# Performance work log

Measured on AMD Instinct MI355X. Metric: run time of the kernel, lower is better.

Reference implementation:

```python
import jax, jax.numpy as jnp
import numpy as np

N_NODES = 100000
N_EDGES = 1600000
IN_F, HID_F, OUT_F, N_CLS = 128, 64, 16, 5
EPS = 1e-12


def _glorot(key, shape):
    fan_in, fan_out = shape[0], shape[1]
    lim = float(np.sqrt(6.0 / (fan_in + fan_out)))
    return jax.random.uniform(key, shape, jnp.float32, -lim, lim)


def setup_inputs() -> dict:
    key = jax.random.key(0)
    ks = jax.random.split(key, 12)
    x = jax.random.normal(ks[0], (N_NODES, IN_F), jnp.float32)
    src = jax.random.randint(ks[1], (N_EDGES,), 0, N_NODES)
    dst = jax.random.randint(ks[2], (N_EDGES,), 0, N_NODES)
    return {
        "x": x, "src": src, "dst": dst,
        # conv1 (SAGEConv pool): fc_pool [in,in]+bias, fc_self/fc_neigh [in,hid] no bias, shared bias
        "pool1_W": _glorot(ks[3], (IN_F, IN_F)), "pool1_b": jnp.zeros((IN_F,), jnp.float32),
        "self1_W": _glorot(ks[4], (IN_F, HID_F)), "neigh1_W": _glorot(ks[5], (IN_F, HID_F)),
        "bias1": jnp.zeros((HID_F,), jnp.float32),
        # conv2
        "pool2_W": _glorot(ks[6], (HID_F, HID_F)), "pool2_b": jnp.zeros((HID_F,), jnp.float32),
        "self2_W": _glorot(ks[7], (HID_F, OUT_F)), "neigh2_W": _glorot(ks[8], (HID_F, OUT_F)),
        "bias2": jnp.zeros((OUT_F,), jnp.float32),
        # edge predictor: Linear(2*out, 5)
        "pred_W": _glorot(ks[9], (2 * OUT_F, N_CLS)), "pred_b": jnp.zeros((N_CLS,), jnp.float32),
    }


def _sage_pool_conv(h, src, dst, Wp, bp, Ws, Wn, b):
    # pool aggregator: m = relu(fc_pool(h)); h_neigh[v] = max over in-edges of m[src]
    m = jax.nn.relu(h @ Wp + bp)                        # [N, d]
    agg = jax.ops.segment_max(m[src], dst, num_segments=h.shape[0])  # [N, d]
    agg = jnp.where(jnp.isneginf(agg), 0.0, agg)        # zero for isolated nodes (DGL behavior)
    return h @ Ws + agg @ Wn + b


def _norm_relu(h):
    # torch F.normalize(p=2, dim=1, eps=1e-12) then relu
    n = jnp.sqrt(jnp.sum(h * h, axis=1, keepdims=True))
    return jax.nn.relu(h / jnp.maximum(n, EPS))


def reference(x, src, dst, pool1_W, pool1_b, self1_W, neigh1_W, bias1,
              pool2_W, pool2_b, self2_W, neigh2_W, bias2, pred_W, pred_b):
    h = _sage_pool_conv(x, src, dst, pool1_W, pool1_b, self1_W, neigh1_W, bias1)
    h = _norm_relu(h)
    h = _sage_pool_conv(h, src, dst, pool2_W, pool2_b, self2_W, neigh2_W, bias2)
    h = _norm_relu(h)                                   # [N, OUT_F]
    # edge scorer: W @ concat(h_u, h_v) + b, split W to avoid materializing concat
    W_u, W_v = pred_W[:OUT_F], pred_W[OUT_F:]
    score = h[src] @ W_u + h[dst] @ W_v + pred_b        # [E, 5]
    return score
```

## Files before the change

kernel.cpp:

```cpp
#include <hip/hip_runtime.h>

#define N_NODES 100000
#define N_EDGES 1600000
constexpr int IN_F = 128, HID_F = 64, OUT_F = 16, N_CLS = 5;

constexpr int NPB = 128;
constexpr int NBK = (N_NODES + NPB - 1) / NPB;
constexpr int BCAP = 2400;
constexpr int FCH = 4096;
constexpr int NCH = (N_EDGES + FCH - 1) / FCH;

typedef __attribute__((ext_vector_type(8))) short bf16x8;
typedef __attribute__((ext_vector_type(4))) float f32x4;
typedef __attribute__((ext_vector_type(2))) unsigned short u16x2;

__device__ __forceinline__ float bf_lo(unsigned u) {
  return __uint_as_float(u << 16);
}
__device__ __forceinline__ float bf_hi(unsigned u) {
  return __uint_as_float(u & 0xffff0000u);
}
__device__ __forceinline__ unsigned f2bf(float f) {
  unsigned u = __float_as_uint(f);
  return (u + 0x7fffu + ((u >> 16) & 1u)) >> 16;
}
__device__ __forceinline__ void unpack8(uint4 u, float* f) {
  f[0] = bf_lo(u.x); f[1] = bf_hi(u.x);
  f[2] = bf_lo(u.y); f[3] = bf_hi(u.y);
  f[4] = bf_lo(u.z); f[5] = bf_hi(u.z);
  f[6] = bf_lo(u.w); f[7] = bf_hi(u.w);
}

__device__ __forceinline__ unsigned pkmax(unsigned a, unsigned b) {
  const u16x2 r = __builtin_elementwise_max(__builtin_bit_cast(u16x2, a),
                                            __builtin_bit_cast(u16x2, b));
  return __builtin_bit_cast(unsigned, r);
}
__device__ __forceinline__ uint4 pkmax4(uint4 a, uint4 b) {
  a.x = pkmax(a.x, b.x);
  a.y = pkmax(a.y, b.y);
  a.z = pkmax(a.z, b.z);
  a.w = pkmax(a.w, b.w);
  return a;
}

template <int K1, int FOUT, bool TWO, bool X1BF, bool X2BF, bool NORM,
          bool YBF>
__global__ __launch_bounds__(256) void node_gemm_mfma(
    const void* __restrict__ X1, const void* __restrict__ X2,
    const float* __restrict__ W1, const float* __restrict__ W2,
    const float* __restrict__ B, void* __restrict__ Y, int n) {
  constexpr int KT = 64;
  constexpr int KT2 = KT / 2;
  constexpr int NT1 = K1 / KT;
  constexpr int NT = TWO ? 2 * NT1 : NT1;
  constexpr int NFT = FOUT / 16;
  constexpr int BM = 64;
  __shared__ unsigned xt[BM * KT2];
  __shared__ unsigned wt[FOUT * KT2];

  const int tid = threadIdx.x;
  const int base = blockIdx.x * BM;
  const int wave = tid >> 6, lane = tid & 63;
  const int l15 = lane & 15, l4 = lane >> 4;

  f32x4 acc[NFT];
#pragma unroll
  for (int nt = 0; nt < NFT; ++nt) {
    const float b = B[nt * 16 + l15];
    acc[nt] = {b, b, b, b};
  }

  for (int t = 0; t < NT; ++t) {
    const bool second = TWO && t >= NT1;
    const int kt0 = (t % NT1) * KT;
#pragma unroll
    for (int q = 0; q < BM * KT2 / 256; ++q) {
      const int idx = tid + q * 256;
      const int r = idx >> 5, c2 = idx & 31;
      const int node = base + r;
      unsigned pk = 0;
      if (node < n) {
        if (second) {
          if (X2BF) {
            pk = reinterpret_cast<const unsigned*>(
                X2)[(size_t)node * (K1 / 2) + kt0 / 2 + c2];
          } else {
            const float2 f2 = reinterpret_cast<const float2*>(
                X2)[(size_t)node * (K1 / 2) + kt0 / 2 + c2];
            pk = f2bf(f2.x) | (f2bf(f2.y) << 16);
          }
        } else {
          if (X1BF) {
            pk = reinterpret_cast<const unsigned*>(
                X1)[(size_t)node * (K1 / 2) + kt0 / 2 + c2];
          } else {
            const float2 f2 = reinterpret_cast<const float2*>(
                X1)[(size_t)node * (K1 / 2) + kt0 / 2 + c2];
            pk = f2bf(f2.x) | (f2bf(f2.y) << 16);
          }
        }
      }
      xt[r * KT2 + (c2 ^ ((r & 7) << 2))] = pk;
    }
    {
      const float* __restrict__ Ws = second ? W2 : W1;
#pragma unroll
      for (int q = 0; q < FOUT * KT2 / 256; ++q) {
        const int idx = tid + q * 256;
        const int c2 = idx / FOUT, f = idx % FOUT;
        const float w0 = Ws[(size_t)(kt0 + 2 * c2) * FOUT + f];
        const float w1 = Ws[(size_t)(kt0 + 2 * c2 + 1) * FOUT + f];
        wt[f * KT2 + (c2 ^ ((f & 7) << 2))] = f2bf(w0) | (f2bf(w1) << 16);
      }
    }
    __syncthreads();
#pragma unroll
    for (int ks = 0; ks < 2; ++ks) {
      const int ar = wave * 16 + l15;
      const bf16x8 af = *reinterpret_cast<const bf16x8*>(
          &xt[ar * KT2 + (((ks * 4 + l4) ^ (l15 & 7)) << 2)]);
#pragma unroll
      for (int nt = 0; nt < NFT; ++nt) {
        const int f = nt * 16 + l15;
        const bf16x8 bfr = *reinterpret_cast<const bf16x8*>(
            &wt[f * KT2 + (((ks * 4 + l4) ^ (l15 & 7)) << 2)]);
        acc[nt] =
            __builtin_amdgcn_mfma_f32_16x16x32_bf16(af, bfr, acc[nt], 0, 0, 0);
      }
    }
    __syncthreads();
  }

  if (NORM) {
    float ss[4] = {0.f, 0.f, 0.f, 0.f};
#pragma unroll
    for (int nt = 0; nt < NFT; ++nt)
#pragma unroll
      for (int r = 0; r < 4; ++r) ss[r] += acc[nt][r] * acc[nt][r];
#pragma unroll
    for (int r = 0; r < 4; ++r) {
#pragma unroll
      for (int off = 1; off < 16; off <<= 1) ss[r] += __shfl_xor(ss[r], off, 16);
      ss[r] = 1.0f / fmaxf(sqrtf(ss[r]), 1e-12f);
    }
#pragma unroll
    for (int nt = 0; nt < NFT; ++nt)
#pragma unroll
      for (int r = 0; r < 4; ++r) acc[nt][r] = fmaxf(acc[nt][r] * ss[r], 0.f);
  } else {
#pragma unroll
    for (int nt = 0; nt < NFT; ++nt)
#pragma unroll
      for (int r = 0; r < 4; ++r) acc[nt][r] = fmaxf(acc[nt][r], 0.f);
  }
#pragma unroll
  for (int r = 0; r < 4; ++r) {
    const int node = base + wave * 16 + l4 * 4 + r;
    if (node < n) {
#pragma unroll
      for (int nt = 0; nt < NFT; ++nt) {
        if (YBF)
          reinterpret_cast<unsigned short*>(Y)[(size_t)node * FOUT + nt * 16 +
                                               l15] =
              (unsigned short)f2bf(acc[nt][r]);
        else
          reinterpret_cast<float*>(Y)[(size_t)node * FOUT + nt * 16 + l15] =
              acc[nt][r];
      }
    }
  }
}

__global__ __launch_bounds__(256) void bucket_fill(
    const int* __restrict__ src, const int* __restrict__ dst,
    int* __restrict__ cursor, unsigned* __restrict__ bedges) {
  __shared__ int hist[NBK];
  __shared__ int bbase[NBK];
  const int tid = threadIdx.x;
  const int c0 = blockIdx.x * FCH;
  const int n4 = (min(FCH, N_EDGES - c0)) >> 2;
  for (int i = tid; i < NBK; i += 256) hist[i] = 0;
  __syncthreads();
  const int4* __restrict__ s4 = reinterpret_cast<const int4*>(src + c0);
  const int4* __restrict__ d4 = reinterpret_cast<const int4*>(dst + c0);
  int4 sv[4], dv[4];
#pragma unroll
  for (int q = 0; q < 4; ++q) {
    const int i = tid + q * 256;
    if (i < n4) {
      sv[q] = s4[i];
      dv[q] = d4[i];
      atomicAdd(&hist[dv[q].x >> 7], 1);
      atomicAdd(&hist[dv[q].y >> 7], 1);
      atomicAdd(&hist[dv[q].z >> 7], 1);
      atomicAdd(&hist[dv[q].w >> 7], 1);
    }
  }
  __syncthreads();
  for (int i = tid; i < NBK; i += 256) {
    const int c = hist[i];
    bbase[i] = c ? atomicAdd(&cursor[i], c) : 0;
    hist[i] = 0;
  }
  __syncthreads();
#pragma unroll
  for (int q = 0; q < 4; ++q) {
    const int i = tid + q * 256;
    if (i < n4) {
#define PUT(dd, ss)                                        \
  {                                                        \
    const int b_ = (dd) >> 7;                              \
    const int r_ = bbase[b_] + atomicAdd(&hist[b_], 1);    \
    if (r_ < BCAP)                                         \
      bedges[(size_t)b_ * BCAP + r_] =                     \
          (unsigned)(ss) | ((unsigned)((dd) & 127) << 20); \
  }
      PUT(dv[q].x, sv[q].x)
      PUT(dv[q].y, sv[q].y)
      PUT(dv[q].z, sv[q].z)
      PUT(dv[q].w, sv[q].w)
#undef PUT
    }
  }
}

__global__ __launch_bounds__(256) void bucket_sort(unsigned* __restrict__ bedges,
                                                   const int* __restrict__ cnt,
                                                   int* __restrict__ ninfo) {
  __shared__ unsigned el[BCAP];
  __shared__ unsigned el2[BCAP];
  __shared__ int hist[NPB];
  __shared__ int csum[NPB];
  __shared__ int posl[NPB];
  const int b = blockIdx.x;
  const int n = min(cnt[b], BCAP);
  unsigned* __restrict__ bp = bedges + (size_t)b * BCAP;
  for (int i = threadIdx.x; i < n; i += 256) el[i] = bp[i];
  for (int i = threadIdx.x; i < NPB; i += 256) hist[i] = 0;
  __syncthreads();
  for (int i = threadIdx.x; i < n; i += 256) atomicAdd(&hist[el[i] >> 20], 1);
  __syncthreads();
  if (threadIdx.x < NPB) csum[threadIdx.x] = hist[threadIdx.x];
  __syncthreads();
  for (int off = 1; off < NPB; off <<= 1) {
    int u = 0;
    if (threadIdx.x < NPB && threadIdx.x >= off) u = csum[threadIdx.x - off];
    __syncthreads();
    if (threadIdx.x < NPB) csum[threadIdx.x] += u;
    __syncthreads();
  }
  if (threadIdx.x < NPB) {
    const int c = hist[threadIdx.x];
    const int beg = csum[threadIdx.x] - c;
    posl[threadIdx.x] = beg;
    const int node = b * NPB + threadIdx.x;
    if (node < N_NODES) ninfo[node] = beg | (c << 12);
  }
  __syncthreads();
  for (int i = threadIdx.x; i < n; i += 256) {
    const unsigned w = el[i];
    const int p = atomicAdd(&posl[w >> 20], 1);
    el2[p] = w & 0xFFFFF;
  }
  __syncthreads();
  for (int i = threadIdx.x; i < n; i += 256) bp[i] = el2[i];
}

template <int LPN>
__global__ __launch_bounds__(256, 8) void gather_max_pk(
    const uint4* __restrict__ M4, const int* __restrict__ ninfo,
    const int* __restrict__ sedges, uint4* __restrict__ A4) {
  constexpr int GPB = 256 / LPN;
  constexpr int UNR = 6;
  const int li = threadIdx.x % LPN;
  const int g0 = blockIdx.x * GPB + threadIdx.x / LPN;
  const int stride = gridDim.x * GPB;
  for (int node = g0; node < N_NODES; node += stride) {
    const int w = ninfo[node];
    const int cnt = w >> 12;
    uint4 a = {0u, 0u, 0u, 0u};
    if (cnt) {
      const int beg = (node >> 7) * BCAP + (w & 0xFFF);
      const int last = beg + cnt - 1;
      for (int j = beg; j <= last; j += UNR) {
        int s[UNR];
#pragma unroll
        for (int q = 0; q < UNR; ++q) s[q] = sedges[min(j + q, last)];
        uint4 u[UNR];
#pragma unroll
        for (int q = 0; q < UNR; ++q) u[q] = M4[(size_t)s[q] * LPN + li];
#pragma unroll
        for (int q = 0; q < UNR; ++q) a = pkmax4(a, u[q]);
      }
    }
    A4[(size_t)node * LPN + li] = a;
  }
}

__global__ __launch_bounds__(256) void edge_score_bf16_kernel(
    const uint4* __restrict__ H, const int* __restrict__ src,
    const int* __restrict__ dst, const float* __restrict__ PW,
    const float* __restrict__ PB, float* __restrict__ OUT) {
  __shared__ float Wl[2 * OUT_F * N_CLS];
  __shared__ float bl[N_CLS];
  if (threadIdx.x < 2 * OUT_F * N_CLS) Wl[threadIdx.x] = PW[threadIdx.x];
  if (threadIdx.x < N_CLS) bl[threadIdx.x] = PB[threadIdx.x];
  __syncthreads();
  for (int e = blockIdx.x * 256 + threadIdx.x; e < N_EDGES;
       e += gridDim.x * 256) {
    const int s = src[e], d = dst[e];
    const uint4 s0 = H[(size_t)s * 2], s1 = H[(size_t)s * 2 + 1];
    const uint4 d0 = H[(size_t)d * 2], d1 = H[(size_t)d * 2 + 1];
    float hs[OUT_F], hd[OUT_F];
    unpack8(s0, hs); unpack8(s1, hs + 8);
    unpack8(d0, hd); unpack8(d1, hd + 8);
    float acc[N_CLS];
#pragma unroll
    for (int c = 0; c < N_CLS; ++c) acc[c] = bl[c];
#pragma unroll
    for (int k = 0; k < OUT_F; ++k) {
#pragma unroll
      for (int c = 0; c < N_CLS; ++c) {
        acc[c] = fmaf(hs[k], Wl[k * N_CLS + c], acc[c]);
        acc[c] = fmaf(hd[k], Wl[(OUT_F + k) * N_CLS + c], acc[c]);
      }
    }
    float* o = OUT + (size_t)e * N_CLS;
#pragma unroll
    for (int c = 0; c < N_CLS; ++c) o[c] = acc[c];
  }
}

extern "C" void kernel_launch(void* const* d_in, const int* in_sizes, int n_in,
                              void* d_out, int out_size, void* d_ws,
                              size_t ws_size, hipStream_t stream) {
  const float* x = (const float*)d_in[0];
  const int* src = (const int*)d_in[1];
  const int* dst = (const int*)d_in[2];
  const float* pool1_W = (const float*)d_in[3];
  const float* pool1_b = (const float*)d_in[4];
  const float* self1_W = (const float*)d_in[5];
  const float* neigh1_W = (const float*)d_in[6];
  const float* bias1 = (const float*)d_in[7];
  const float* pool2_W = (const float*)d_in[8];
  const float* pool2_b = (const float*)d_in[9];
  const float* self2_W = (const float*)d_in[10];
  const float* neigh2_W = (const float*)d_in[11];
  const float* bias2 = (const float*)d_in[12];
  const float* pred_W = (const float*)d_in[13];
  const float* pred_b = (const float*)d_in[14];
  float* out = (float*)d_out;

  int* cursor = (int*)d_ws;
  int* ninfo = cursor + 1024;
  unsigned* bedges = (unsigned*)(ninfo + 100352);
  char* bufA = (char*)(bedges + (size_t)NBK * BCAP);
  char* bufB = bufA + 25600000;
  void* m1 = (void*)bufA;
  void* agg1 = (void*)bufB;
  void* h1 = (void*)bufA;
  void* m2 = (void*)bufB;
  void* agg2 = (void*)(bufA + 12800000);
  void* h2 = (void*)bufB;

  hipMemsetAsync(cursor, 0, 1024 * sizeof(int), stream);
  bucket_fill<<<NCH, 256, 0, stream>>>(src, dst, cursor, bedges);
  bucket_sort<<<NBK, 256, 0, stream>>>(bedges, cursor, ninfo);

  const int ngrid = (N_NODES + 63) / 64;

  node_gemm_mfma<IN_F, IN_F, false, false, false, false, true>
      <<<ngrid, 256, 0, stream>>>(x, nullptr, pool1_W, nullptr, pool1_b, m1,
                                  N_NODES);
  gather_max_pk<16><<<2048, 256, 0, stream>>>(
      (const uint4*)m1, ninfo, (const int*)bedges, (uint4*)agg1);
  node_gemm_mfma<IN_F, HID_F, true, false, true, true, true>
      <<<ngrid, 256, 0, stream>>>(x, agg1, self1_W, neigh1_W, bias1, h1,
                                  N_NODES);

  node_gemm_mfma<HID_F, HID_F, false, true, false, false, true>
      <<<ngrid, 256, 0, stream>>>(h1, nullptr, pool2_W, nullptr, pool2_b, m2,
                                  N_NODES);
  gather_max_pk<8><<<2048, 256, 0, stream>>>(
      (const uint4*)m2, ninfo, (const int*)bedges, (uint4*)agg2);
  node_gemm_mfma<HID_F, OUT_F, true, true, true, true, true>
      <<<ngrid, 256, 0, stream>>>(h1, agg2, self2_W, neigh2_W, bias2, h2,
                                  N_NODES);

  edge_score_bf16_kernel<<<4096, 256, 0, stream>>>((const uint4*)h2, src, dst,
                                                   pred_W, pred_b, out);
}
```

Baseline: 238.5 us.

## Store pool outputs in feature planes and gather per plane for locality

The pool GEMMs now write their bf16 output as 16-feature planes, each node's 32 bytes contiguous within a plane, instead of row-major. A new gather kernel assigns each block one plane and 128 nodes, with two lanes per node. With 8 consecutive blocks covering the same nodes across planes, each plane's working set (about 3.2 MB) is meant to fit better in L2 and the MI355X CDNA4 cache hierarchy during the random gathers. The cost is more blocks, more ninfo and edge-index reads (once per plane), and smaller 32-byte gather granules.

```diff
diff --git a/kernel.cpp b/kernel.cpp
--- a/kernel.cpp
+++ b/kernel.cpp
@@ -45,7 +45,7 @@
 }
 
 template <int K1, int FOUT, bool TWO, bool X1BF, bool X2BF, bool NORM,
-          bool YBF>
+          bool YBF, bool YPLANE>
 __global__ __launch_bounds__(256) void node_gemm_mfma(
     const void* __restrict__ X1, const void* __restrict__ X2,
     const float* __restrict__ W1, const float* __restrict__ W2,
@@ -160,13 +160,16 @@
     if (node < n) {
 #pragma unroll
       for (int nt = 0; nt < NFT; ++nt) {
-        if (YBF)
-          reinterpret_cast<unsigned short*>(Y)[(size_t)node * FOUT + nt * 16 +
-                                               l15] =
+        if (YBF) {
+          const size_t idx = YPLANE
+                                 ? ((size_t)nt * n + node) * 16 + l15
+                                 : (size_t)node * FOUT + nt * 16 + l15;
+          reinterpret_cast<unsigned short*>(Y)[idx] =
               (unsigned short)f2bf(acc[nt][r]);
-        else
+        } else {
           reinterpret_cast<float*>(Y)[(size_t)node * FOUT + nt * 16 + l15] =
               acc[nt][r];
+        }
       }
     }
   }
@@ -267,35 +270,37 @@
   for (int i = threadIdx.x; i < n; i += 256) bp[i] = el2[i];
 }
 
-template <int LPN>
-__global__ __launch_bounds__(256, 8) void gather_max_pk(
-    const uint4* __restrict__ M4, const int* __restrict__ ninfo,
+template <int NPLANES, int NSUB>
+__global__ __launch_bounds__(256) void plane_gather_max(
+    const uint4* __restrict__ MP, const int* __restrict__ ninfo,
     const int* __restrict__ sedges, uint4* __restrict__ A4) {
-  constexpr int GPB = 256 / LPN;
-  constexpr int UNR = 6;
-  const int li = threadIdx.x % LPN;
-  const int g0 = blockIdx.x * GPB + threadIdx.x / LPN;
-  const int stride = gridDim.x * GPB;
-  for (int node = g0; node < N_NODES; node += stride) {
-    const int w = ninfo[node];
-    const int cnt = w >> 12;
-    uint4 a = {0u, 0u, 0u, 0u};
-    if (cnt) {
-      const int beg = (node >> 7) * BCAP + (w & 0xFFF);
-      const int last = beg + cnt - 1;
-      for (int j = beg; j <= last; j += UNR) {
-        int s[UNR];
-#pragma unroll
-        for (int q = 0; q < UNR; ++q) s[q] = sedges[min(j + q, last)];
-        uint4 u[UNR];
-#pragma unroll
-        for (int q = 0; q < UNR; ++q) u[q] = M4[(size_t)s[q] * LPN + li];
-#pragma unroll
-        for (int q = 0; q < UNR; ++q) a = pkmax4(a, u[q]);
-      }
-    }
-    A4[(size_t)node * LPN + li] = a;
-  }
+  constexpr int UNR = 8;
+  const int s = blockIdx.x & 7;
+  const int chunk = blockIdx.x >> 3;
+  const int plane = s % NPLANES;
+  const int sub = s / NPLANES;
+  const int node = chunk * (128 * NSUB) + sub * 128 + (threadIdx.x >> 1);
+  const int li = threadIdx.x & 1;
+  if (node >= N_NODES) return;
+  const uint4* __restrict__ P = MP + (size_t)plane * N_NODES * 2;
+  const int w = ninfo[node];
+  const int cnt = w >> 12;
+  uint4 a = {0u, 0u, 0u, 0u};
+  if (cnt) {
+    const int beg = (node >> 7) * BCAP + (w & 0xFFF);
+    const int last = beg + cnt - 1;
+    for (int j = beg; j <= last; j += UNR) {
+      int ss[UNR];
+#pragma unroll
+      for (int q = 0; q < UNR; ++q) ss[q] = sedges[min(j + q, last)];
+      uint4 u[UNR];
+#pragma unroll
+      for (int q = 0; q < UNR; ++q) u[q] = P[(size_t)ss[q] * 2 + li];
+#pragma unroll
+      for (int q = 0; q < UNR; ++q) a = pkmax4(a, u[q]);
+    }
+  }
+  A4[(size_t)node * (NPLANES * 2) + plane * 2 + li] = a;
 }
 
 __global__ __launch_bounds__(256) void edge_score_bf16_kernel(
@@ -369,22 +374,24 @@
   bucket_sort<<<NBK, 256, 0, stream>>>(bedges, cursor, ninfo);
 
   const int ngrid = (N_NODES + 63) / 64;
-
-  node_gemm_mfma<IN_F, IN_F, false, false, false, false, true>
+  const int gchunks1 = (N_NODES + 127) / 128;
+  const int gchunks2 = (N_NODES + 255) / 256;
+
+  node_gemm_mfma<IN_F, IN_F, false, false, false, false, true, true>
       <<<ngrid, 256, 0, stream>>>(x, nullptr, pool1_W, nullptr, pool1_b, m1,
                                   N_NODES);
-  gather_max_pk<16><<<2048, 256, 0, stream>>>(
+  plane_gather_max<8, 1><<<gchunks1 * 8, 256, 0, stream>>>(
       (const uint4*)m1, ninfo, (const int*)bedges, (uint4*)agg1);
-  node_gemm_mfma<IN_F, HID_F, true, false, true, true, true>
+  node_gemm_mfma<IN_F, HID_F, true, false, true, true, true, false>
       <<<ngrid, 256, 0, stream>>>(x, agg1, self1_W, neigh1_W, bias1, h1,
                                   N_NODES);
 
-  node_gemm_mfma<HID_F, HID_F, false, true, false, false, true>
+  node_gemm_mfma<HID_F, HID_F, false, true, false, false, true, true>
       <<<ngrid, 256, 0, stream>>>(h1, nullptr, pool2_W, nullptr, pool2_b, m2,
                                   N_NODES);
-  gather_max_pk<8><<<2048, 256, 0, stream>>>(
+  plane_gather_max<4, 2><<<gchunks2 * 8, 256, 0, stream>>>(
       (const uint4*)m2, ninfo, (const int*)bedges, (uint4*)agg2);
-  node_gemm_mfma<HID_F, OUT_F, true, true, true, true, true>
+  node_gemm_mfma<HID_F, OUT_F, true, true, true, true, true, false>
       <<<ngrid, 256, 0, stream>>>(h1, agg2, self2_W, neigh2_W, bias2, h2,
                                   N_NODES);
 
```

Measured after the change: 294.6 us. 23.5% more time.

## Fuse self-projection into pool GEMM to avoid re-reading node features

Applied to the files above, without the earlier changes.

The pool-projection GEMM now also computes the self-projection (h @ Ws) in the same pass over the node features, storing it as bf16 in scratch space borrowed from the output buffer. The combine kernel then only multiplies the aggregated features by Wn, adds the stored self term, and applies normalize and ReLU. This removes a second read of x (fp32, 128 wide) and of h1, at the cost of writing and re-reading an extra bf16 intermediate and a wider weight tile in shared memory. Rounding the self term to bf16 before the add slightly changes numerics.

```diff
diff --git a/kernel.cpp b/kernel.cpp
--- a/kernel.cpp
+++ b/kernel.cpp
@@ -19,6 +19,9 @@
 }
 __device__ __forceinline__ float bf_hi(unsigned u) {
   return __uint_as_float(u & 0xffff0000u);
+}
+__device__ __forceinline__ float us2f(unsigned short u) {
+  return __uint_as_float(((unsigned)u) << 16);
 }
 __device__ __forceinline__ unsigned f2bf(float f) {
   unsigned u = __float_as_uint(f);
@@ -44,20 +47,20 @@
   return a;
 }
 
-template <int K1, int FOUT, bool TWO, bool X1BF, bool X2BF, bool NORM,
-          bool YBF>
-__global__ __launch_bounds__(256) void node_gemm_mfma(
-    const void* __restrict__ X1, const void* __restrict__ X2,
-    const float* __restrict__ W1, const float* __restrict__ W2,
-    const float* __restrict__ B, void* __restrict__ Y, int n) {
+template <int K1, int F1, int F2, bool XBF>
+__global__ __launch_bounds__(256) void dense_dual_mfma(
+    const void* __restrict__ X, const float* __restrict__ W1,
+    const float* __restrict__ W2, const float* __restrict__ B,
+    void* __restrict__ Y1, void* __restrict__ Y2, int n) {
   constexpr int KT = 64;
   constexpr int KT2 = KT / 2;
-  constexpr int NT1 = K1 / KT;
-  constexpr int NT = TWO ? 2 * NT1 : NT1;
-  constexpr int NFT = FOUT / 16;
+  constexpr int NT = K1 / KT;
+  constexpr int FT = F1 + F2;
+  constexpr int NFT = FT / 16;
+  constexpr int NF1 = F1 / 16;
   constexpr int BM = 64;
   __shared__ unsigned xt[BM * KT2];
-  __shared__ unsigned wt[FOUT * KT2];
+  __shared__ unsigned wt[FT * KT2];
 
   const int tid = threadIdx.x;
   const int base = blockIdx.x * BM;
@@ -67,13 +70,12 @@
   f32x4 acc[NFT];
 #pragma unroll
   for (int nt = 0; nt < NFT; ++nt) {
-    const float b = B[nt * 16 + l15];
+    const float b = (nt < NF1) ? B[nt * 16 + l15] : 0.f;
     acc[nt] = {b, b, b, b};
   }
 
   for (int t = 0; t < NT; ++t) {
-    const bool second = TWO && t >= NT1;
-    const int kt0 = (t % NT1) * KT;
+    const int kt0 = t * KT;
 #pragma unroll
     for (int q = 0; q < BM * KT2 / 256; ++q) {
       const int idx = tid + q * 256;
@@ -81,38 +83,30 @@
       const int node = base + r;
       unsigned pk = 0;
       if (node < n) {
-        if (second) {
-          if (X2BF) {
-            pk = reinterpret_cast<const unsigned*>(
-                X2)[(size_t)node * (K1 / 2) + kt0 / 2 + c2];
-          } else {
-            const float2 f2 = reinterpret_cast<const float2*>(
-                X2)[(size_t)node * (K1 / 2) + kt0 / 2 + c2];
-            pk = f2bf(f2.x) | (f2bf(f2.y) << 16);
-          }
+        if (XBF) {
+          pk = reinterpret_cast<const unsigned*>(
+              X)[(size_t)node * (K1 / 2) + kt0 / 2 + c2];
         } else {
-          if (X1BF) {
-            pk = reinterpret_cast<const unsigned*>(
-                X1)[(size_t)node * (K1 / 2) + kt0 / 2 + c2];
-          } else {
-            const float2 f2 = reinterpret_cast<const float2*>(
-                X1)[(size_t)node * (K1 / 2) + kt0 / 2 + c2];
-            pk = f2bf(f2.x) | (f2bf(f2.y) << 16);
-          }
+          const float2 f2 = reinterpret_cast<const float2*>(
+              X)[(size_t)node * (K1 / 2) + kt0 / 2 + c2];
+          pk = f2bf(f2.x) | (f2bf(f2.y) << 16);
         }
       }
       xt[r * KT2 + (c2 ^ ((r & 7) << 2))] = pk;
     }
-    {
-      const float* __restrict__ Ws = second ? W2 : W1;
-#pragma unroll
-      for (int q = 0; q < FOUT * KT2 / 256; ++q) {
-        const int idx = tid + q * 256;
-        const int c2 = idx / FOUT, f = idx % FOUT;
-        const float w0 = Ws[(size_t)(kt0 + 2 * c2) * FOUT + f];
-        const float w1 = Ws[(size_t)(kt0 + 2 * c2 + 1) * FOUT + f];
-        wt[f * KT2 + (c2 ^ ((f & 7) << 2))] = f2bf(w0) | (f2bf(w1) << 16);
-      }
+#pragma unroll
+    for (int q = 0; q < FT * KT2 / 256; ++q) {
+      const int idx = tid + q * 256;
+      const int c2 = idx / FT, f = idx % FT;
+      float w0, w1;
+      if (f < F1) {
+        w0 = W1[(size_t)(kt0 + 2 * c2) * F1 + f];
+        w1 = W1[(size_t)(kt0 + 2 * c2 + 1) * F1 + f];
+      } else {
+        w0 = W2[(size_t)(kt0 + 2 * c2) * F2 + (f - F1)];
+        w1 = W2[(size_t)(kt0 + 2 * c2 + 1) * F2 + (f - F1)];
+      }
+      wt[f * KT2 + (c2 ^ ((f & 7) << 2))] = f2bf(w0) | (f2bf(w1) << 16);
     }
     __syncthreads();
 #pragma unroll
@@ -132,41 +126,119 @@
     __syncthreads();
   }
 
-  if (NORM) {
-    float ss[4] = {0.f, 0.f, 0.f, 0.f};
-#pragma unroll
-    for (int nt = 0; nt < NFT; ++nt)
-#pragma unroll
-      for (int r = 0; r < 4; ++r) ss[r] += acc[nt][r] * acc[nt][r];
-#pragma unroll
-    for (int r = 0; r < 4; ++r) {
-#pragma unroll
-      for (int off = 1; off < 16; off <<= 1) ss[r] += __shfl_xor(ss[r], off, 16);
-      ss[r] = 1.0f / fmaxf(sqrtf(ss[r]), 1e-12f);
-    }
-#pragma unroll
-    for (int nt = 0; nt < NFT; ++nt)
-#pragma unroll
-      for (int r = 0; r < 4; ++r) acc[nt][r] = fmaxf(acc[nt][r] * ss[r], 0.f);
-  } else {
-#pragma unroll
-    for (int nt = 0; nt < NFT; ++nt)
-#pragma unroll
-      for (int r = 0; r < 4; ++r) acc[nt][r] = fmaxf(acc[nt][r], 0.f);
-  }
 #pragma unroll
   for (int r = 0; r < 4; ++r) {
     const int node = base + wave * 16 + l4 * 4 + r;
     if (node < n) {
 #pragma unroll
       for (int nt = 0; nt < NFT; ++nt) {
-        if (YBF)
-          reinterpret_cast<unsigned short*>(Y)[(size_t)node * FOUT + nt * 16 +
-                                               l15] =
+        if (nt < NF1) {
+          reinterpret_cast<unsigned short*>(Y1)[(size_t)node * F1 + nt * 16 +
+                                                l15] =
+              (unsigned short)f2bf(fmaxf(acc[nt][r], 0.f));
+        } else {
+          reinterpret_cast<unsigned short*>(Y2)[(size_t)node * F2 +
+                                                (nt - NF1) * 16 + l15] =
               (unsigned short)f2bf(acc[nt][r]);
-        else
-          reinterpret_cast<float*>(Y)[(size_t)node * FOUT + nt * 16 + l15] =
-              acc[nt][r];
+        }
+      }
+    }
+  }
+}
+
+template <int K1, int FOUT>
+__global__ __launch_bounds__(256) void combine_mfma(
+    const void* __restrict__ AGG, const float* __restrict__ Wn,
+    const float* __restrict__ B, const unsigned short* __restrict__ S,
+    void* __restrict__ Y, int n) {
+  constexpr int KT = 64;
+  constexpr int KT2 = KT / 2;
+  constexpr int NT = K1 / KT;
+  constexpr int NFT = FOUT / 16;
+  constexpr int BM = 64;
+  __shared__ unsigned xt[BM * KT2];
+  __shared__ unsigned wt[FOUT * KT2];
+
+  const int tid = threadIdx.x;
+  const int base = blockIdx.x * BM;
+  const int wave = tid >> 6, lane = tid & 63;
+  const int l15 = lane & 15, l4 = lane >> 4;
+
+  f32x4 acc[NFT];
+#pragma unroll
+  for (int nt = 0; nt < NFT; ++nt) {
+    const float b = B[nt * 16 + l15];
+    acc[nt] = {b, b, b, b};
+  }
+
+  for (int t = 0; t < NT; ++t) {
+    const int kt0 = t * KT;
+#pragma unroll
+    for (int q = 0; q < BM * KT2 / 256; ++q) {
+      const int idx = tid + q * 256;
+      const int r = idx >> 5, c2 = idx & 31;
+      const int node = base + r;
+      unsigned pk = 0;
+      if (node < n)
+        pk = reinterpret_cast<const unsigned*>(
+            AGG)[(size_t)node * (K1 / 2) + kt0 / 2 + c2];
+      xt[r * KT2 + (c2 ^ ((r & 7) << 2))] = pk;
+    }
+#pragma unroll
+    for (int q = 0; q < FOUT * KT2 / 256; ++q) {
+      const int idx = tid + q * 256;
+      const int c2 = idx / FOUT, f = idx % FOUT;
+      const float w0 = Wn[(size_t)(kt0 + 2 * c2) * FOUT + f];
+      const float w1 = Wn[(size_t)(kt0 + 2 * c2 + 1) * FOUT + f];
+      wt[f * KT2 + (c2 ^ ((f & 7) << 2))] = f2bf(w0) | (f2bf(w1) << 16);
+    }
+    __syncthreads();
+#pragma unroll
+    for (int ks = 0; ks < 2; ++ks) {
+      const int ar = wave * 16 + l15;
+      const bf16x8 af = *reinterpret_cast<const bf16x8*>(
+          &xt[ar * KT2 + (((ks * 4 + l4) ^ (l15 & 7)) << 2)]);
+#pragma unroll
+      for (int nt = 0; nt < NFT; ++nt) {
+        const int f = nt * 16 + l15;
+        const bf16x8 bfr = *reinterpret_cast<const bf16x8*>(
+            &wt[f * KT2 + (((ks * 4 + l4) ^ (l15 & 7)) << 2)]);
+        acc[nt] =
+            __builtin_amdgcn_mfma_f32_16x16x32_bf16(af, bfr, acc[nt], 0, 0, 0);
+      }
+    }
+    __syncthreads();
+  }
+
+#pragma unroll
+  for (int r = 0; r < 4; ++r) {
+    const int node = base + wave * 16 + l4 * 4 + r;
+    if (node < n) {
+#pragma unroll
+      for (int nt = 0; nt < NFT; ++nt)
+        acc[nt][r] += us2f(S[(size_t)node * FOUT + nt * 16 + l15]);
+    }
+  }
+  float ss[4] = {0.f, 0.f, 0.f, 0.f};
+#pragma unroll
+  for (int nt = 0; nt < NFT; ++nt)
+#pragma unroll
+    for (int r = 0; r < 4; ++r) ss[r] += acc[nt][r] * acc[nt][r];
+#pragma unroll
+  for (int r = 0; r < 4; ++r) {
+#pragma unroll
+    for (int off = 1; off < 16; off <<= 1) ss[r] += __shfl_xor(ss[r], off, 16);
+    ss[r] = 1.0f / fmaxf(sqrtf(ss[r]), 1e-12f);
+  }
+#pragma unroll
+  for (int r = 0; r < 4; ++r) {
+    const int node = base + wave * 16 + l4 * 4 + r;
+    if (node < n) {
+#pragma unroll
+      for (int nt = 0; nt < NFT; ++nt) {
+        reinterpret_cast<unsigned short*>(Y)[(size_t)node * FOUT + nt * 16 +
+                                             l15] =
+            (unsigned short)f2bf(fmaxf(acc[nt][r] * ss[r], 0.f));
       }
     }
   }
@@ -362,7 +434,10 @@
   void* h1 = (void*)bufA;
   void* m2 = (void*)bufB;
   void* agg2 = (void*)(bufA + 12800000);
-  void* h2 = (void*)bufB;
+  void* h2 = (void*)(bufB + 12800000);
+  unsigned short* s1 = (unsigned short*)d_out;
+  unsigned short* s2 =
+      (unsigned short*)((char*)d_out + 12800000);
 
   hipMemsetAsync(cursor, 0, 1024 * sizeof(int), stream);
   bucket_fill<<<NCH, 256, 0, stream>>>(src, dst, cursor, bedges);
@@ -370,23 +445,19 @@
 
   const int ngrid = (N_NODES + 63) / 64;
 
-  node_gemm_mfma<IN_F, IN_F, false, false, false, false, true>
-      <<<ngrid, 256, 0, stream>>>(x, nullptr, pool1_W, nullptr, pool1_b, m1,
-                                  N_NODES);
+  dense_dual_mfma<IN_F, IN_F, HID_F, false><<<ngrid, 256, 0, stream>>>(
+      x, pool1_W, self1_W, pool1_b, m1, s1, N_NODES);
   gather_max_pk<16><<<2048, 256, 0, stream>>>(
       (const uint4*)m1, ninfo, (const int*)bedges, (uint4*)agg1);
-  node_gemm_mfma<IN_F, HID_F, true, false, true, true, true>
-      <<<ngrid, 256, 0, stream>>>(x, agg1, self1_W, neigh1_W, bias1, h1,
-                                  N_NODES);
-
-  node_gemm_mfma<HID_F, HID_F, false, true, false, false, true>
-      <<<ngrid, 256, 0, stream>>>(h1, nullptr, pool2_W, nullptr, pool2_b, m2,
-                                  N_NODES);
+  combine_mfma<IN_F, HID_F><<<ngrid, 256, 0, stream>>>(
+      agg1, neigh1_W, bias1, s1, h1, N_NODES);
+
+  dense_dual_mfma<HID_F, HID_F, OUT_F, true><<<ngrid, 256, 0, stream>>>(
+      h1, pool2_W, self2_W, pool2_b, m2, s2, N_NODES);
   gather_max_pk<8><<<2048, 256, 0, stream>>>(
       (const uint4*)m2, ninfo, (const int*)bedges, (uint4*)agg2);
-  node_gemm_mfma<HID_F, OUT_F, true, true, true, true, true>
-      <<<ngrid, 256, 0, stream>>>(h1, agg2, self2_W, neigh2_W, bias2, h2,
-                                  N_NODES);
+  combine_mfma<HID_F, OUT_F><<<ngrid, 256, 0, stream>>>(
+      agg2, neigh2_W, bias2, s2, h2, N_NODES);
 
   edge_score_bf16_kernel<<<4096, 256, 0, stream>>>((const uint4*)h2, src, dst,
                                                    pred_W, pred_b, out);
```

New measurement: 307.5 us. 1.29x slower.

## Precompute per-node edge-score projections and stage coalesced edge output via LDS

Applied to the files above, without the earlier changes.

The layer-2 combine kernel now also computes per-node projections h@W_u+b and h@W_v (stored as a 16-float padded row). The edge kernel then only adds two 5-float vectors per edge instead of running a 32x5 matvec on gathered bf16 features. Outputs are staged in shared memory so each block writes them as coalesced float4 stores. The bucket_fill chunk size is also halved to launch more blocks, and the fp32 UV layout raises per-edge gather bytes slightly.

```diff
diff --git a/kernel.cpp b/kernel.cpp
--- a/kernel.cpp
+++ b/kernel.cpp
@@ -7,7 +7,7 @@
 constexpr int NPB = 128;
 constexpr int NBK = (N_NODES + NPB - 1) / NPB;
 constexpr int BCAP = 2400;
-constexpr int FCH = 4096;
+constexpr int FCH = 2048;
 constexpr int NCH = (N_EDGES + FCH - 1) / FCH;
 
 typedef __attribute__((ext_vector_type(8))) short bf16x8;
@@ -20,15 +20,12 @@
 __device__ __forceinline__ float bf_hi(unsigned u) {
   return __uint_as_float(u & 0xffff0000u);
 }
+__device__ __forceinline__ float us2f(unsigned short u) {
+  return __uint_as_float(((unsigned)u) << 16);
+}
 __device__ __forceinline__ unsigned f2bf(float f) {
   unsigned u = __float_as_uint(f);
   return (u + 0x7fffu + ((u >> 16) & 1u)) >> 16;
-}
-__device__ __forceinline__ void unpack8(uint4 u, float* f) {
-  f[0] = bf_lo(u.x); f[1] = bf_hi(u.x);
-  f[2] = bf_lo(u.y); f[3] = bf_hi(u.y);
-  f[4] = bf_lo(u.z); f[5] = bf_hi(u.z);
-  f[6] = bf_lo(u.w); f[7] = bf_hi(u.w);
 }
 
 __device__ __forceinline__ unsigned pkmax(unsigned a, unsigned b) {
@@ -172,11 +169,103 @@
   }
 }
 
+__global__ __launch_bounds__(256) void combine2_uv_mfma(
+    const void* __restrict__ X1, const void* __restrict__ X2,
+    const float* __restrict__ W1, const float* __restrict__ W2,
+    const float* __restrict__ B, const float* __restrict__ PW,
+    const float* __restrict__ PB, float* __restrict__ UV, int n) {
+  constexpr int K1 = HID_F, FOUT = OUT_F;
+  constexpr int KT = 64, KT2 = 32, BM = 64;
+  __shared__ unsigned xt[BM * KT2];
+  __shared__ unsigned wt[FOUT * KT2];
+  __shared__ float wl[2 * OUT_F * N_CLS];
+
+  const int tid = threadIdx.x;
+  const int base = blockIdx.x * BM;
+  const int wave = tid >> 6, lane = tid & 63;
+  const int l15 = lane & 15, l4 = lane >> 4;
+
+  f32x4 acc = {B[l15], B[l15], B[l15], B[l15]};
+
+  for (int t = 0; t < 2; ++t) {
+    const void* __restrict__ Xs = t ? X2 : X1;
+#pragma unroll
+    for (int q = 0; q < BM * KT2 / 256; ++q) {
+      const int idx = tid + q * 256;
+      const int r = idx >> 5, c2 = idx & 31;
+      const int node = base + r;
+      unsigned pk = 0;
+      if (node < n)
+        pk = reinterpret_cast<const unsigned*>(
+            Xs)[(size_t)node * (K1 / 2) + c2];
+      xt[r * KT2 + (c2 ^ ((r & 7) << 2))] = pk;
+    }
+    {
+      const float* __restrict__ Ws = t ? W2 : W1;
+#pragma unroll
+      for (int q = 0; q < FOUT * KT2 / 256; ++q) {
+        const int idx = tid + q * 256;
+        const int c2 = idx / FOUT, f = idx % FOUT;
+        const float w0 = Ws[(size_t)(2 * c2) * FOUT + f];
+        const float w1 = Ws[(size_t)(2 * c2 + 1) * FOUT + f];
+        wt[f * KT2 + (c2 ^ ((f & 7) << 2))] = f2bf(w0) | (f2bf(w1) << 16);
+      }
+    }
+    __syncthreads();
+#pragma unroll
+    for (int ks = 0; ks < 2; ++ks) {
+      const int ar = wave * 16 + l15;
+      const bf16x8 af = *reinterpret_cast<const bf16x8*>(
+          &xt[ar * KT2 + (((ks * 4 + l4) ^ (l15 & 7)) << 2)]);
+      const bf16x8 bfr = *reinterpret_cast<const bf16x8*>(
+          &wt[l15 * KT2 + (((ks * 4 + l4) ^ (l15 & 7)) << 2)]);
+      acc = __builtin_amdgcn_mfma_f32_16x16x32_bf16(af, bfr, acc, 0, 0, 0);
+    }
+    __syncthreads();
+  }
+
+  if (tid < 2 * OUT_F * N_CLS) wl[tid] = PW[tid];
+
+  float ss[4];
+#pragma unroll
+  for (int r = 0; r < 4; ++r) ss[r] = acc[r] * acc[r];
+#pragma unroll
+  for (int r = 0; r < 4; ++r) {
+#pragma unroll
+    for (int off = 1; off < 16; off <<= 1) ss[r] += __shfl_xor(ss[r], off, 16);
+    ss[r] = 1.0f / fmaxf(sqrtf(ss[r]), 1e-12f);
+  }
+
+  float* ht = reinterpret_cast<float*>(xt);
+#pragma unroll
+  for (int r = 0; r < 4; ++r) {
+    const int row = wave * 16 + l4 * 4 + r;
+    const float h = fmaxf(acc[r] * ss[r], 0.f);
+    ht[row * 17 + l15] = us2f((unsigned short)f2bf(h));
+  }
+  __syncthreads();
+
+  for (int it = tid; it < BM * 10; it += 256) {
+    const int nl = it / 10, j = it % 10;
+    const int node = base + nl;
+    if (node < n) {
+      const int jc = (j < 5) ? j : j - 5;
+      const int kb = (j < 5) ? 0 : 16;
+      float s = (j < 5) ? PB[j] : 0.f;
+#pragma unroll
+      for (int k = 0; k < 16; ++k)
+        s = fmaf(ht[nl * 17 + k], wl[(kb + k) * 5 + jc], s);
+      UV[(size_t)node * 16 + ((j < 5) ? j : j + 3)] = s;
+    }
+  }
+}
+
 __global__ __launch_bounds__(256) void bucket_fill(
     const int* __restrict__ src, const int* __restrict__ dst,
     int* __restrict__ cursor, unsigned* __restrict__ bedges) {
   __shared__ int hist[NBK];
   __shared__ int bbase[NBK];
+  constexpr int NQ = FCH / 1024;
   const int tid = threadIdx.x;
   const int c0 = blockIdx.x * FCH;
   const int n4 = (min(FCH, N_EDGES - c0)) >> 2;
@@ -184,9 +273,9 @@
   __syncthreads();
   const int4* __restrict__ s4 = reinterpret_cast<const int4*>(src + c0);
   const int4* __restrict__ d4 = reinterpret_cast<const int4*>(dst + c0);
-  int4 sv[4], dv[4];
-#pragma unroll
-  for (int q = 0; q < 4; ++q) {
+  int4 sv[NQ], dv[NQ];
+#pragma unroll
+  for (int q = 0; q < NQ; ++q) {
     const int i = tid + q * 256;
     if (i < n4) {
       sv[q] = s4[i];
@@ -205,7 +294,7 @@
   }
   __syncthreads();
 #pragma unroll
-  for (int q = 0; q < 4; ++q) {
+  for (int q = 0; q < NQ; ++q) {
     const int i = tid + q * 256;
     if (i < n4) {
 #define PUT(dd, ss)                                        \
@@ -298,37 +387,29 @@
   }
 }
 
-__global__ __launch_bounds__(256) void edge_score_bf16_kernel(
-    const uint4* __restrict__ H, const int* __restrict__ src,
-    const int* __restrict__ dst, const float* __restrict__ PW,
-    const float* __restrict__ PB, float* __restrict__ OUT) {
-  __shared__ float Wl[2 * OUT_F * N_CLS];
-  __shared__ float bl[N_CLS];
-  if (threadIdx.x < 2 * OUT_F * N_CLS) Wl[threadIdx.x] = PW[threadIdx.x];
-  if (threadIdx.x < N_CLS) bl[threadIdx.x] = PB[threadIdx.x];
-  __syncthreads();
-  for (int e = blockIdx.x * 256 + threadIdx.x; e < N_EDGES;
-       e += gridDim.x * 256) {
+__global__ __launch_bounds__(256) void edge_score_uv(
+    const float* __restrict__ UV, const int* __restrict__ src,
+    const int* __restrict__ dst, float* __restrict__ OUT) {
+  __shared__ float ob[256 * N_CLS];
+  constexpr int NCHK = N_EDGES / 256;
+  for (int chunk = blockIdx.x; chunk < NCHK; chunk += gridDim.x) {
+    const int e = chunk * 256 + threadIdx.x;
     const int s = src[e], d = dst[e];
-    const uint4 s0 = H[(size_t)s * 2], s1 = H[(size_t)s * 2 + 1];
-    const uint4 d0 = H[(size_t)d * 2], d1 = H[(size_t)d * 2 + 1];
-    float hs[OUT_F], hd[OUT_F];
-    unpack8(s0, hs); unpack8(s1, hs + 8);
-    unpack8(d0, hd); unpack8(d1, hd + 8);
-    float acc[N_CLS];
-#pragma unroll
-    for (int c = 0; c < N_CLS; ++c) acc[c] = bl[c];
-#pragma unroll
-    for (int k = 0; k < OUT_F; ++k) {
-#pragma unroll
-      for (int c = 0; c < N_CLS; ++c) {
-        acc[c] = fmaf(hs[k], Wl[k * N_CLS + c], acc[c]);
-        acc[c] = fmaf(hd[k], Wl[(OUT_F + k) * N_CLS + c], acc[c]);
-      }
-    }
-    float* o = OUT + (size_t)e * N_CLS;
-#pragma unroll
-    for (int c = 0; c < N_CLS; ++c) o[c] = acc[c];
+    const float4 u0 = *reinterpret_cast<const float4*>(UV + (size_t)s * 16);
+    const float u4 = UV[(size_t)s * 16 + 4];
+    const float4 v0 =
+        *reinterpret_cast<const float4*>(UV + (size_t)d * 16 + 8);
+    const float v4 = UV[(size_t)d * 16 + 12];
+    ob[threadIdx.x * 5 + 0] = u0.x + v0.x;
+    ob[threadIdx.x * 5 + 1] = u0.y + v0.y;
+    ob[threadIdx.x * 5 + 2] = u0.z + v0.z;
+    ob[threadIdx.x * 5 + 3] = u0.w + v0.w;
+    ob[threadIdx.x * 5 + 4] = u4 + v4;
+    __syncthreads();
+    float4* o4 = reinterpret_cast<float4*>(OUT + (size_t)chunk * 1280);
+    const float4* ob4 = reinterpret_cast<const float4*>(ob);
+    for (int i = threadIdx.x; i < 320; i += 256) o4[i] = ob4[i];
+    __syncthreads();
   }
 }
 
@@ -362,7 +443,7 @@
   void* h1 = (void*)bufA;
   void* m2 = (void*)bufB;
   void* agg2 = (void*)(bufA + 12800000);
-  void* h2 = (void*)bufB;
+  float* uv = (float*)(bufB + 12800000);
 
   hipMemsetAsync(cursor, 0, 1024 * sizeof(int), stream);
   bucket_fill<<<NCH, 256, 0, stream>>>(src, dst, cursor, bedges);
@@ -384,10 +465,9 @@
                                   N_NODES);
   gather_max_pk<8><<<2048, 256, 0, stream>>>(
       (const uint4*)m2, ninfo, (const int*)bedges, (uint4*)agg2);
-  node_gemm_mfma<HID_F, OUT_F, true, true, true, true, true>
-      <<<ngrid, 256, 0, stream>>>(h1, agg2, self2_W, neigh2_W, bias2, h2,
-                                  N_NODES);
-
-  edge_score_bf16_kernel<<<4096, 256, 0, stream>>>((const uint4*)h2, src, dst,
-                                                   pred_W, pred_b, out);
-}
+  combine2_uv_mfma<<<ngrid, 256, 0, stream>>>(h1, agg2, self2_W, neigh2_W,
+                                              bias2, pred_W, pred_b, uv,
+                                              N_NODES);
+
+  edge_score_uv<<<2048, 256, 0, stream>>>(uv, src, dst, out);
+}
```

Measured after the change: 256.4 us. 7.5% more time.
